# Kernel optimization log

Hardware: AMD Instinct MI355X
Metric: run time of the kernel (lower is better)

## Reference

```python
import jax, jax.numpy as jnp
import numpy as np

NEG_INF = -1.0e15  # matches the module's self.infty


def setup_inputs() -> dict:
    key = jax.random.key(0)
    ks = jax.random.split(key, 12)
    B, N, D, H, HD = 256, 1024, 128, 8, 16
    inp = {
        "x": jax.random.normal(ks[0], (B, N, D), dtype=jnp.float32),
        "h_g": jax.random.normal(ks[1], (B, D), dtype=jnp.float32),
        "first": jax.random.normal(ks[2], (B, D), dtype=jnp.float32),
        "last": jax.random.normal(ks[3], (B, D), dtype=jnp.float32),
        "context": jax.random.normal(ks[4], (B, 2), dtype=jnp.float32),
        "K": jax.random.normal(ks[5], (B, H, N, HD), dtype=jnp.float32),
        "V": jax.random.normal(ks[6], (B, H, N, HD), dtype=jnp.float32),
        "K_lg": jax.random.normal(ks[7], (B, N, D), dtype=jnp.float32),
        "Wq": jax.random.normal(ks[8], (D, 3 * D + 2), dtype=jnp.float32) * 0.05,
        "bq": jnp.zeros((D,), dtype=jnp.float32),
        "Wo": jax.random.normal(ks[9], (D, D), dtype=jnp.float32) * 0.05,
        "bo": jnp.zeros((D,), dtype=jnp.float32),
        "mask": jax.random.randint(ks[10], (B, N), 0, 2, dtype=jnp.int32),
        "t": 1,
    }
    return inp


def reference(x, h_g, first, last, context, K, V, K_lg, Wq, bq, Wo, bo, mask, t):
    B, N, D = x.shape
    H, HD = K.shape[1], K.shape[3]
    # t > 0 path: context vector from graph embedding + first/last visited nodes
    h_c = jnp.concatenate([h_g, first, last, context], axis=1)  # [B, 3D+2]
    Q = h_c @ Wq.T + bq                                          # [B, D]
    Q = Q.reshape(B, H, HD)                                      # single query per head
    # masked single-query multi-head attention
    scale = jnp.sqrt(jnp.asarray(HD, dtype=x.dtype))
    scores = jnp.einsum("bhd,bhnd->bhn", Q, K) / scale          # [B, H, N]
    scores = jnp.where(mask[:, None, :] == 0, NEG_INF, scores)
    attn = jax.nn.softmax(scores, axis=-1)
    u = jnp.einsum("bhn,bhnd->bhd", attn, V).reshape(B, D)       # [B, D]
    u = u @ Wo.T + bo
    # pointer logits with tanh clipping
    logits = jnp.einsum("bd,bnd->bn", u, K_lg) / jnp.sqrt(jnp.asarray(D, dtype=x.dtype))
    logits = 10.0 * jnp.tanh(logits)
    logits = jnp.where(mask == 0, NEG_INF, logits)
    p = jax.nn.softmax(logits, axis=1)                           # [B, N]
    vertexes = jnp.argmax(p, axis=1)[:, None]                    # greedy (sample=False)
    probs = jnp.take_along_axis(p, vertexes, axis=1)             # [B, 1]
    return vertexes, probs
```

## Files before the change

### kernel.cpp

```cpp
#include <hip/hip_runtime.h>
#include <math.h>

#define Bn 256
#define Nn 1024
#define Dn 128
#define Hn 8
#define HDn 16
#define NEG_INF -1.0e15f

__global__ __launch_bounds__(128) void k_q(
    const float* __restrict__ h_g, const float* __restrict__ first,
    const float* __restrict__ last, const float* __restrict__ context,
    const float* __restrict__ Wq, const float* __restrict__ bq,
    float* __restrict__ Qout)
{
    __shared__ __align__(16) float hc[3 * Dn + 2];
    const int b = blockIdx.x;
    const int t = threadIdx.x;
    hc[t]          = h_g[b * Dn + t];
    hc[Dn + t]     = first[b * Dn + t];
    hc[2 * Dn + t] = last[b * Dn + t];
    if (t < 2) hc[3 * Dn + t] = context[b * 2 + t];
    __syncthreads();

    const float2* w2 = (const float2*)(Wq + (size_t)t * (3 * Dn + 2));
    const float2* h2 = (const float2*)hc;
    float acc = bq[t];
#pragma unroll 8
    for (int k = 0; k < (3 * Dn + 2) / 2; ++k) {
        float2 w = w2[k], h = h2[k];
        acc = fmaf(w.x, h.x, fmaf(w.y, h.y, acc));
    }
    Qout[b * Dn + t] = acc;
}

__global__ __launch_bounds__(256) void k_attn(
    const float* __restrict__ Q, const float* __restrict__ K,
    const float* __restrict__ V, const int* __restrict__ mask,
    float* __restrict__ Uout)
{
    __shared__ float sQ[HDn];
    __shared__ __align__(16) int sM[Nn];
    __shared__ float sRed[4];
    __shared__ float sSum[4];
    __shared__ float sUp[4][HDn];

    const int bh = blockIdx.x;
    const int b = bh >> 3;
    const int tid = threadIdx.x;
    const int lane = tid & 63, wave = tid >> 6;
    const int d4 = tid & 3;
    const int g = tid >> 2;

    ((int4*)sM)[tid] = ((const int4*)(mask + (size_t)b * Nn))[tid];
    if (tid < HDn) sQ[tid] = Q[b * Dn + (bh & 7) * HDn + tid];
    __syncthreads();
    const float4 qf = ((const float4*)sQ)[d4];

    const float4* __restrict__ Kp = (const float4*)(K + (size_t)bh * Nn * HDn);
    const float4* __restrict__ Vp = (const float4*)(V + (size_t)bh * Nn * HDn);

    float4 kf[16], vf[16];
#pragma unroll
    for (int i = 0; i < 16; ++i) kf[i] = Kp[(size_t)(g + 64 * i) * 4 + d4];
#pragma unroll
    for (int i = 0; i < 16; ++i) vf[i] = Vp[(size_t)(g + 64 * i) * 4 + d4];
    __builtin_amdgcn_sched_barrier(0);

    float s[16];
    float lmax = NEG_INF;
#pragma unroll
    for (int i = 0; i < 16; ++i) {
        float p = qf.x * kf[i].x + qf.y * kf[i].y + qf.z * kf[i].z + qf.w * kf[i].w;
        p += __shfl_xor(p, 1, 64);
        p += __shfl_xor(p, 2, 64);
        p = (sM[g + 64 * i] == 0) ? NEG_INF : (p * 0.25f);
        s[i] = p;
        lmax = fmaxf(lmax, p);
    }
#pragma unroll
    for (int o = 4; o <= 32; o <<= 1) lmax = fmaxf(lmax, __shfl_xor(lmax, o, 64));
    if (lane == 0) sRed[wave] = lmax;
    __syncthreads();
    const float m = fmaxf(fmaxf(sRed[0], sRed[1]), fmaxf(sRed[2], sRed[3]));

    float lsum = 0.f;
    float4 acc = {0.f, 0.f, 0.f, 0.f};
#pragma unroll
    for (int i = 0; i < 16; ++i) {
        const float e = __expf(s[i] - m);
        lsum += e;
        acc.x = fmaf(e, vf[i].x, acc.x);
        acc.y = fmaf(e, vf[i].y, acc.y);
        acc.z = fmaf(e, vf[i].z, acc.z);
        acc.w = fmaf(e, vf[i].w, acc.w);
    }
#pragma unroll
    for (int o = 4; o <= 32; o <<= 1) {
        acc.x += __shfl_xor(acc.x, o, 64);
        acc.y += __shfl_xor(acc.y, o, 64);
        acc.z += __shfl_xor(acc.z, o, 64);
        acc.w += __shfl_xor(acc.w, o, 64);
        lsum  += __shfl_xor(lsum, o, 64);
    }
    if (lane < 4) {
        sUp[wave][lane * 4 + 0] = acc.x;
        sUp[wave][lane * 4 + 1] = acc.y;
        sUp[wave][lane * 4 + 2] = acc.z;
        sUp[wave][lane * 4 + 3] = acc.w;
    }
    if (lane == 0) sSum[wave] = lsum;
    __syncthreads();
    if (tid < HDn) {
        const float inv = 1.0f / (sSum[0] + sSum[1] + sSum[2] + sSum[3]);
        const float u = (sUp[0][tid] + sUp[1][tid] + sUp[2][tid] + sUp[3][tid]) * inv;
        Uout[b * Dn + (bh & 7) * HDn + tid] = u;
    }
}

__global__ __launch_bounds__(1024) void k_ptr(
    const float* __restrict__ U, const float* __restrict__ Wo,
    const float* __restrict__ bo, const float* __restrict__ K_lg,
    const int* __restrict__ mask, float* __restrict__ out)
{
    __shared__ __align__(16) float sU[Dn];
    __shared__ __align__(16) float sU2[Dn];
    __shared__ __align__(16) float sL[Nn];
    __shared__ float sRv[16];
    __shared__ int   sRi[16];
    __shared__ float sRs[16];

    const int b = blockIdx.x;
    const int tid = threadIdx.x;
    const int lane = tid & 63, wave = tid >> 6;

    if (tid < Dn) sU[tid] = U[b * Dn + tid];
    __syncthreads();
    {
        const int d = tid >> 3, e8 = tid & 7;
        const float4* wrow = (const float4*)(Wo + (size_t)d * Dn + e8 * 16);
        const float4* su4 = (const float4*)(sU + e8 * 16);
        float acc = 0.f;
#pragma unroll
        for (int k = 0; k < 4; ++k) {
            const float4 w = wrow[k], u = su4[k];
            acc = fmaf(w.x, u.x, fmaf(w.y, u.y, fmaf(w.z, u.z, fmaf(w.w, u.w, acc))));
        }
        acc += __shfl_xor(acc, 1, 64);
        acc += __shfl_xor(acc, 2, 64);
        acc += __shfl_xor(acc, 4, 64);
        if (e8 == 0) sU2[d] = acc + bo[d];
    }
    __syncthreads();

    const float4* __restrict__ Kl = (const float4*)(K_lg + (size_t)b * Nn * Dn);
    const int* __restrict__ mrow = mask + (size_t)b * Nn;
    const int grp = tid >> 5, l32 = tid & 31;
    const float4 u2f = ((const float4*)sU2)[l32];
    const float sc = 0.08838834764831845f;
#pragma unroll
    for (int it0 = 0; it0 < 32; it0 += 4) {
        float4 kl[4];
#pragma unroll
        for (int j = 0; j < 4; ++j)
            kl[j] = Kl[(size_t)(grp + 32 * (it0 + j)) * 32 + l32];
        __builtin_amdgcn_sched_barrier(0);
#pragma unroll
        for (int j = 0; j < 4; ++j) {
            float p = kl[j].x * u2f.x + kl[j].y * u2f.y + kl[j].z * u2f.z + kl[j].w * u2f.w;
#pragma unroll
            for (int o = 16; o >= 1; o >>= 1) p += __shfl_xor(p, o, 64);
            if (l32 == 0) {
                const int n = grp + 32 * (it0 + j);
                sL[n] = (mrow[n] == 0) ? NEG_INF : 10.0f * tanhf(p * sc);
            }
        }
    }
    __syncthreads();

    float bv = sL[tid]; int bi = tid;
#pragma unroll
    for (int o = 32; o >= 1; o >>= 1) {
        const float ov = __shfl_xor(bv, o, 64);
        const int oi = __shfl_xor(bi, o, 64);
        if (ov > bv || (ov == bv && oi < bi)) { bv = ov; bi = oi; }
    }
    if (lane == 0) { sRv[wave] = bv; sRi[wave] = bi; }
    __syncthreads();
    bv = sRv[0]; bi = sRi[0];
#pragma unroll
    for (int w = 1; w < 16; ++w) {
        const float ov = sRv[w]; const int oi = sRi[w];
        if (ov > bv || (ov == bv && oi < bi)) { bv = ov; bi = oi; }
    }

    float lsum = __expf(sL[tid] - bv);
#pragma unroll
    for (int o = 32; o >= 1; o >>= 1) lsum += __shfl_xor(lsum, o, 64);
    if (lane == 0) sRs[wave] = lsum;
    __syncthreads();
    if (tid == 0) {
        float tot = 0.f;
#pragma unroll
        for (int w = 0; w < 16; ++w) tot += sRs[w];
        out[b] = (float)bi;
        out[Bn + b] = 1.0f / tot;
    }
}

extern "C" void kernel_launch(void* const* d_in, const int* in_sizes, int n_in,
                              void* d_out, int out_size, void* d_ws, size_t ws_size,
                              hipStream_t stream) {
    const float* h_g     = (const float*)d_in[1];
    const float* first   = (const float*)d_in[2];
    const float* last    = (const float*)d_in[3];
    const float* context = (const float*)d_in[4];
    const float* K       = (const float*)d_in[5];
    const float* V       = (const float*)d_in[6];
    const float* K_lg    = (const float*)d_in[7];
    const float* Wq      = (const float*)d_in[8];
    const float* bq      = (const float*)d_in[9];
    const float* Wo      = (const float*)d_in[10];
    const float* bo      = (const float*)d_in[11];
    const int*   mask    = (const int*)d_in[12];
    float* out = (float*)d_out;

    float* Qws = (float*)d_ws;
    float* Uws = Qws + Bn * Dn;

    k_q   <<<Bn,      128, 0, stream>>>(h_g, first, last, context, Wq, bq, Qws);
    k_attn<<<Bn * Hn, 256, 0, stream>>>(Qws, K, V, mask, Uws);
    k_ptr <<<Bn,     1024, 0, stream>>>(Uws, Wo, bo, K_lg, mask, out);
}
```

Baseline: 113.2 us.

## Restructure attention kernel: thread-per-key rows, four heads per block, double-buffered loads

```diff
diff --git a/kernel.cpp b/kernel.cpp
--- a/kernel.cpp
+++ b/kernel.cpp
@@ -34,87 +34,106 @@
     Qout[b * Dn + t] = acc;
 }
 
-__global__ __launch_bounds__(256) void k_attn(
+__global__ __launch_bounds__(512, 4) void k_attn(
     const float* __restrict__ Q, const float* __restrict__ K,
     const float* __restrict__ V, const int* __restrict__ mask,
     float* __restrict__ Uout)
 {
-    __shared__ float sQ[HDn];
-    __shared__ __align__(16) int sM[Nn];
-    __shared__ float sRed[4];
+    __shared__ float sQ[64];
+    __shared__ float sPart[512][17];
+    __shared__ float sOut[64];
     __shared__ float sSum[4];
-    __shared__ float sUp[4][HDn];
-
-    const int bh = blockIdx.x;
-    const int b = bh >> 3;
+
+    const int blk = blockIdx.x;
+    const int b = blk >> 1, pr = blk & 1;
     const int tid = threadIdx.x;
-    const int lane = tid & 63, wave = tid >> 6;
-    const int d4 = tid & 3;
-    const int g = tid >> 2;
-
-    ((int4*)sM)[tid] = ((const int4*)(mask + (size_t)b * Nn))[tid];
-    if (tid < HDn) sQ[tid] = Q[b * Dn + (bh & 7) * HDn + tid];
-    __syncthreads();
-    const float4 qf = ((const float4*)sQ)[d4];
-
-    const float4* __restrict__ Kp = (const float4*)(K + (size_t)bh * Nn * HDn);
-    const float4* __restrict__ Vp = (const float4*)(V + (size_t)bh * Nn * HDn);
-
-    float4 kf[16], vf[16];
-#pragma unroll
-    for (int i = 0; i < 16; ++i) kf[i] = Kp[(size_t)(g + 64 * i) * 4 + d4];
-#pragma unroll
-    for (int i = 0; i < 16; ++i) vf[i] = Vp[(size_t)(g + 64 * i) * 4 + d4];
-    __builtin_amdgcn_sched_barrier(0);
-
-    float s[16];
-    float lmax = NEG_INF;
-#pragma unroll
-    for (int i = 0; i < 16; ++i) {
-        float p = qf.x * kf[i].x + qf.y * kf[i].y + qf.z * kf[i].z + qf.w * kf[i].w;
-        p += __shfl_xor(p, 1, 64);
-        p += __shfl_xor(p, 2, 64);
-        p = (sM[g + 64 * i] == 0) ? NEG_INF : (p * 0.25f);
-        s[i] = p;
-        lmax = fmaxf(lmax, p);
-    }
-#pragma unroll
-    for (int o = 4; o <= 32; o <<= 1) lmax = fmaxf(lmax, __shfl_xor(lmax, o, 64));
-    if (lane == 0) sRed[wave] = lmax;
-    __syncthreads();
-    const float m = fmaxf(fmaxf(sRed[0], sRed[1]), fmaxf(sRed[2], sRed[3]));
-
-    float lsum = 0.f;
-    float4 acc = {0.f, 0.f, 0.f, 0.f};
-#pragma unroll
-    for (int i = 0; i < 16; ++i) {
-        const float e = __expf(s[i] - m);
-        lsum += e;
-        acc.x = fmaf(e, vf[i].x, acc.x);
-        acc.y = fmaf(e, vf[i].y, acc.y);
-        acc.z = fmaf(e, vf[i].z, acc.z);
-        acc.w = fmaf(e, vf[i].w, acc.w);
-    }
-#pragma unroll
-    for (int o = 4; o <= 32; o <<= 1) {
-        acc.x += __shfl_xor(acc.x, o, 64);
-        acc.y += __shfl_xor(acc.y, o, 64);
-        acc.z += __shfl_xor(acc.z, o, 64);
-        acc.w += __shfl_xor(acc.w, o, 64);
-        lsum  += __shfl_xor(lsum, o, 64);
-    }
-    if (lane < 4) {
-        sUp[wave][lane * 4 + 0] = acc.x;
-        sUp[wave][lane * 4 + 1] = acc.y;
-        sUp[wave][lane * 4 + 2] = acc.z;
-        sUp[wave][lane * 4 + 3] = acc.w;
-    }
-    if (lane == 0) sSum[wave] = lsum;
-    __syncthreads();
-    if (tid < HDn) {
-        const float inv = 1.0f / (sSum[0] + sSum[1] + sSum[2] + sSum[3]);
-        const float u = (sUp[0][tid] + sUp[1][tid] + sUp[2][tid] + sUp[3][tid]) * inv;
-        Uout[b * Dn + (bh & 7) * HDn + tid] = u;
+    const int hl = tid >> 7;
+    const int h = pr * 4 + hl;
+    const int lh = tid & 127;
+
+    if (tid < 64) sQ[tid] = Q[b * Dn + pr * 64 + tid];
+
+    const int* __restrict__ mrow = mask + (size_t)b * Nn;
+    int mk[8];
+#pragma unroll
+    for (int i = 0; i < 8; ++i) mk[i] = mrow[lh + 128 * i];
+
+    __syncthreads();
+    float4 q4[4];
+#pragma unroll
+    for (int j = 0; j < 4; ++j) q4[j] = ((const float4*)(sQ + hl * 16))[j];
+
+    const float4* __restrict__ Kp = (const float4*)(K + ((size_t)b * Hn + h) * Nn * HDn);
+    const float4* __restrict__ Vp = (const float4*)(V + ((size_t)b * Hn + h) * Nn * HDn);
+
+    float4 kb[2][4], vb[2][4];
+#pragma unroll
+    for (int j = 0; j < 4; ++j) {
+        kb[0][j] = Kp[(size_t)lh * 4 + j];
+        vb[0][j] = Vp[(size_t)lh * 4 + j];
+    }
+
+    float4 u0 = {0,0,0,0}, u1 = {0,0,0,0}, u2 = {0,0,0,0}, u3 = {0,0,0,0};
+    float sum = 0.f;
+
+#pragma unroll
+    for (int i = 0; i < 8; ++i) {
+        const int cur = i & 1, nxt = cur ^ 1;
+        if (i < 7) {
+            const int n = lh + 128 * (i + 1);
+#pragma unroll
+            for (int j = 0; j < 4; ++j) {
+                kb[nxt][j] = Kp[(size_t)n * 4 + j];
+                vb[nxt][j] = Vp[(size_t)n * 4 + j];
+            }
+        }
+        __builtin_amdgcn_sched_barrier(0);
+        float s = 0.f;
+#pragma unroll
+        for (int j = 0; j < 4; ++j) {
+            s = fmaf(q4[j].x, kb[cur][j].x, s);
+            s = fmaf(q4[j].y, kb[cur][j].y, s);
+            s = fmaf(q4[j].z, kb[cur][j].z, s);
+            s = fmaf(q4[j].w, kb[cur][j].w, s);
+        }
+        const float e = mk[i] ? __expf(s * 0.25f) : 0.f;
+        sum += e;
+        u0.x = fmaf(e, vb[cur][0].x, u0.x); u0.y = fmaf(e, vb[cur][0].y, u0.y);
+        u0.z = fmaf(e, vb[cur][0].z, u0.z); u0.w = fmaf(e, vb[cur][0].w, u0.w);
+        u1.x = fmaf(e, vb[cur][1].x, u1.x); u1.y = fmaf(e, vb[cur][1].y, u1.y);
+        u1.z = fmaf(e, vb[cur][1].z, u1.z); u1.w = fmaf(e, vb[cur][1].w, u1.w);
+        u2.x = fmaf(e, vb[cur][2].x, u2.x); u2.y = fmaf(e, vb[cur][2].y, u2.y);
+        u2.z = fmaf(e, vb[cur][2].z, u2.z); u2.w = fmaf(e, vb[cur][2].w, u2.w);
+        u3.x = fmaf(e, vb[cur][3].x, u3.x); u3.y = fmaf(e, vb[cur][3].y, u3.y);
+        u3.z = fmaf(e, vb[cur][3].z, u3.z); u3.w = fmaf(e, vb[cur][3].w, u3.w);
+    }
+
+    {
+        float* p = sPart[tid];
+        p[0]=u0.x; p[1]=u0.y; p[2]=u0.z; p[3]=u0.w;
+        p[4]=u1.x; p[5]=u1.y; p[6]=u1.z; p[7]=u1.w;
+        p[8]=u2.x; p[9]=u2.y; p[10]=u2.z; p[11]=u2.w;
+        p[12]=u3.x; p[13]=u3.y; p[14]=u3.z; p[15]=u3.w;
+        p[16]=sum;
+    }
+    __syncthreads();
+
+    if (tid < 64) {
+        const int hh = tid >> 4, d = tid & 15;
+        float a = 0.f;
+#pragma unroll 8
+        for (int j = 0; j < 128; ++j) a += sPart[hh * 128 + j][d];
+        sOut[tid] = a;
+    } else if (tid < 68) {
+        const int hh = tid - 64;
+        float a = 0.f;
+#pragma unroll 8
+        for (int j = 0; j < 128; ++j) a += sPart[hh * 128 + j][16];
+        sSum[hh] = a;
+    }
+    __syncthreads();
+    if (tid < 64) {
+        Uout[b * Dn + pr * 64 + tid] = sOut[tid] / sSum[tid >> 4];
     }
 }
 
@@ -229,6 +248,6 @@
     float* Uws = Qws + Bn * Dn;
 
     k_q   <<<Bn,      128, 0, stream>>>(h_g, first, last, context, Wq, bq, Qws);
-    k_attn<<<Bn * Hn, 256, 0, stream>>>(Qws, K, V, mask, Uws);
+    k_attn<<<Bn * 2,  512, 0, stream>>>(Qws, K, V, mask, Uws);
     k_ptr <<<Bn,     1024, 0, stream>>>(Uws, Wo, bo, K_lg, mask, out);
 }
```

Result: slower. 117.4 us (+3.7%).

## Stream K/V through double-buffered LDS via global_load_lds in attention kernel

Applied to the files above, without the earlier changes.

```diff
diff --git a/kernel.cpp b/kernel.cpp
--- a/kernel.cpp
+++ b/kernel.cpp
@@ -7,6 +7,15 @@
 #define Hn 8
 #define HDn 16
 #define NEG_INF -1.0e15f
+
+#define AS(n) __attribute__((address_space(n)))
+#define WAITV(n) asm volatile("s_waitcnt vmcnt(" #n ")" ::: "memory")
+
+__device__ __forceinline__ void gl_lds16(const float* g, float* l) {
+    __builtin_amdgcn_global_load_lds(
+        (AS(1) void*)(unsigned long long)g,
+        (AS(3) void*)l, 16, 0, 0);
+}
 
 __global__ __launch_bounds__(128) void k_q(
     const float* __restrict__ h_g, const float* __restrict__ first,
@@ -39,82 +48,95 @@
     const float* __restrict__ V, const int* __restrict__ mask,
     float* __restrict__ Uout)
 {
-    __shared__ float sQ[HDn];
-    __shared__ __align__(16) int sM[Nn];
-    __shared__ float sRed[4];
-    __shared__ float sSum[4];
-    __shared__ float sUp[4][HDn];
+    __shared__ __align__(16) float sK[2 * 2048];
+    __shared__ __align__(16) float sV[2 * 2048];
+    __shared__ __align__(16) float sP[16 * 4];
+    __shared__ float sS[4];
 
     const int bh = blockIdx.x;
-    const int b = bh >> 3;
+    const int b = bh >> 3, h = bh & 7;
     const int tid = threadIdx.x;
     const int lane = tid & 63, wave = tid >> 6;
-    const int d4 = tid & 3;
-    const int g = tid >> 2;
-
-    ((int4*)sM)[tid] = ((const int4*)(mask + (size_t)b * Nn))[tid];
-    if (tid < HDn) sQ[tid] = Q[b * Dn + (bh & 7) * HDn + tid];
-    __syncthreads();
-    const float4 qf = ((const float4*)sQ)[d4];
-
-    const float4* __restrict__ Kp = (const float4*)(K + (size_t)bh * Nn * HDn);
-    const float4* __restrict__ Vp = (const float4*)(V + (size_t)bh * Nn * HDn);
-
-    float4 kf[16], vf[16];
-#pragma unroll
-    for (int i = 0; i < 16; ++i) kf[i] = Kp[(size_t)(g + 64 * i) * 4 + d4];
-#pragma unroll
-    for (int i = 0; i < 16; ++i) vf[i] = Vp[(size_t)(g + 64 * i) * 4 + d4];
+    const int g = tid & 3;
+    const int kq = tid >> 2;
+
+    const int* __restrict__ mrow = mask + (size_t)b * Nn;
+    int mk[16];
+#pragma unroll
+    for (int c = 0; c < 8; ++c) {
+        mk[c * 2]     = mrow[c * 128 + kq];
+        mk[c * 2 + 1] = mrow[c * 128 + 64 + kq];
+    }
+    const float4 qg = ((const float4*)(Q + (size_t)b * Dn + h * HDn))[g];
+    WAITV(0);
     __builtin_amdgcn_sched_barrier(0);
 
-    float s[16];
-    float lmax = NEG_INF;
-#pragma unroll
-    for (int i = 0; i < 16; ++i) {
-        float p = qf.x * kf[i].x + qf.y * kf[i].y + qf.z * kf[i].z + qf.w * kf[i].w;
-        p += __shfl_xor(p, 1, 64);
-        p += __shfl_xor(p, 2, 64);
-        p = (sM[g + 64 * i] == 0) ? NEG_INF : (p * 0.25f);
-        s[i] = p;
-        lmax = fmaxf(lmax, p);
-    }
-#pragma unroll
-    for (int o = 4; o <= 32; o <<= 1) lmax = fmaxf(lmax, __shfl_xor(lmax, o, 64));
-    if (lane == 0) sRed[wave] = lmax;
-    __syncthreads();
-    const float m = fmaxf(fmaxf(sRed[0], sRed[1]), fmaxf(sRed[2], sRed[3]));
-
-    float lsum = 0.f;
-    float4 acc = {0.f, 0.f, 0.f, 0.f};
-#pragma unroll
-    for (int i = 0; i < 16; ++i) {
-        const float e = __expf(s[i] - m);
-        lsum += e;
-        acc.x = fmaf(e, vf[i].x, acc.x);
-        acc.y = fmaf(e, vf[i].y, acc.y);
-        acc.z = fmaf(e, vf[i].z, acc.z);
-        acc.w = fmaf(e, vf[i].w, acc.w);
-    }
+    const float4* __restrict__ Kg = (const float4*)(K + (size_t)bh * Nn * HDn);
+    const float4* __restrict__ Vg = (const float4*)(V + (size_t)bh * Nn * HDn);
+
+#define STAGE(c, buf) {                                                       \
+    gl_lds16((const float*)(Kg + (c) * 512 + tid),       sK + (buf) * 2048 + tid * 4);        \
+    gl_lds16((const float*)(Kg + (c) * 512 + 256 + tid), sK + (buf) * 2048 + 1024 + tid * 4); \
+    gl_lds16((const float*)(Vg + (c) * 512 + tid),       sV + (buf) * 2048 + tid * 4);        \
+    gl_lds16((const float*)(Vg + (c) * 512 + 256 + tid), sV + (buf) * 2048 + 1024 + tid * 4); \
+}
+
+    STAGE(0, 0);
+    STAGE(1, 1);
+
+    float4 u = {0.f, 0.f, 0.f, 0.f};
+    float sum = 0.f;
+
+#pragma unroll
+    for (int c = 0; c < 8; ++c) {
+        if (c < 7) { WAITV(4); } else { WAITV(0); }
+        __builtin_amdgcn_sched_barrier(0);
+        __builtin_amdgcn_s_barrier();
+        const float* kb = sK + (c & 1) * 2048;
+        const float* vb = sV + (c & 1) * 2048;
+#pragma unroll
+        for (int kk = 0; kk < 2; ++kk) {
+            const int key = kq + 64 * kk;
+            const float4 kf = *(const float4*)(kb + key * 16 + g * 4);
+            const float4 vf = *(const float4*)(vb + key * 16 + g * 4);
+            float p = qg.x * kf.x + qg.y * kf.y + qg.z * kf.z + qg.w * kf.w;
+            p += __shfl_xor(p, 1, 64);
+            p += __shfl_xor(p, 2, 64);
+            const float e = mk[c * 2 + kk] ? __expf(p * 0.25f) : 0.f;
+            sum += e;
+            u.x = fmaf(e, vf.x, u.x);
+            u.y = fmaf(e, vf.y, u.y);
+            u.z = fmaf(e, vf.z, u.z);
+            u.w = fmaf(e, vf.w, u.w);
+        }
+        __builtin_amdgcn_s_barrier();
+        if (c < 6) STAGE(c + 2, c & 1);
+    }
+#undef STAGE
+
 #pragma unroll
     for (int o = 4; o <= 32; o <<= 1) {
-        acc.x += __shfl_xor(acc.x, o, 64);
-        acc.y += __shfl_xor(acc.y, o, 64);
-        acc.z += __shfl_xor(acc.z, o, 64);
-        acc.w += __shfl_xor(acc.w, o, 64);
-        lsum  += __shfl_xor(lsum, o, 64);
-    }
-    if (lane < 4) {
-        sUp[wave][lane * 4 + 0] = acc.x;
-        sUp[wave][lane * 4 + 1] = acc.y;
-        sUp[wave][lane * 4 + 2] = acc.z;
-        sUp[wave][lane * 4 + 3] = acc.w;
-    }
-    if (lane == 0) sSum[wave] = lsum;
-    __syncthreads();
-    if (tid < HDn) {
-        const float inv = 1.0f / (sSum[0] + sSum[1] + sSum[2] + sSum[3]);
-        const float u = (sUp[0][tid] + sUp[1][tid] + sUp[2][tid] + sUp[3][tid]) * inv;
-        Uout[b * Dn + (bh & 7) * HDn + tid] = u;
+        u.x += __shfl_xor(u.x, o, 64);
+        u.y += __shfl_xor(u.y, o, 64);
+        u.z += __shfl_xor(u.z, o, 64);
+        u.w += __shfl_xor(u.w, o, 64);
+        sum += __shfl_xor(sum, o, 64);
+    }
+    if (lane < 4) ((float4*)sP)[wave * 4 + lane] = u;
+    if (lane == 0) sS[wave] = sum;
+    __syncthreads();
+    if (tid < 4) {
+        const float4 t0 = ((const float4*)sP)[0 * 4 + tid];
+        const float4 t1 = ((const float4*)sP)[1 * 4 + tid];
+        const float4 t2 = ((const float4*)sP)[2 * 4 + tid];
+        const float4 t3 = ((const float4*)sP)[3 * 4 + tid];
+        const float inv = 1.0f / (sS[0] + sS[1] + sS[2] + sS[3]);
+        float4 r;
+        r.x = (t0.x + t1.x + t2.x + t3.x) * inv;
+        r.y = (t0.y + t1.y + t2.y + t3.y) * inv;
+        r.z = (t0.z + t1.z + t2.z + t3.z) * inv;
+        r.w = (t0.w + t1.w + t2.w + t3.w) * inv;
+        ((float4*)(Uout + (size_t)b * Dn + h * HDn))[tid] = r;
     }
 }
 
```

Result: no change. 113.6 us (+0.3%).

## Restructure attention to one block per batch and drop softmax max pass

Applied to the files above, without the earlier changes.

```diff
diff --git a/kernel.cpp b/kernel.cpp
--- a/kernel.cpp
+++ b/kernel.cpp
@@ -7,6 +7,8 @@
 #define Hn 8
 #define HDn 16
 #define NEG_INF -1.0e15f
+
+typedef float v4f __attribute__((ext_vector_type(4)));
 
 __global__ __launch_bounds__(128) void k_q(
     const float* __restrict__ h_g, const float* __restrict__ first,
@@ -34,87 +36,80 @@
     Qout[b * Dn + t] = acc;
 }
 
-__global__ __launch_bounds__(256) void k_attn(
+__global__ __launch_bounds__(1024) void k_attn(
     const float* __restrict__ Q, const float* __restrict__ K,
     const float* __restrict__ V, const int* __restrict__ mask,
     float* __restrict__ Uout)
 {
-    __shared__ float sQ[HDn];
-    __shared__ __align__(16) int sM[Nn];
-    __shared__ float sRed[4];
-    __shared__ float sSum[4];
-    __shared__ float sUp[4][HDn];
-
-    const int bh = blockIdx.x;
-    const int b = bh >> 3;
+    __shared__ __align__(16) float sPart[16][Hn][20];
+    __shared__ __align__(16) float sTot[Hn][20];
+
+    const int b = blockIdx.x;
     const int tid = threadIdx.x;
     const int lane = tid & 63, wave = tid >> 6;
-    const int d4 = tid & 3;
-    const int g = tid >> 2;
-
-    ((int4*)sM)[tid] = ((const int4*)(mask + (size_t)b * Nn))[tid];
-    if (tid < HDn) sQ[tid] = Q[b * Dn + (bh & 7) * HDn + tid];
-    __syncthreads();
-    const float4 qf = ((const float4*)sQ)[d4];
-
-    const float4* __restrict__ Kp = (const float4*)(K + (size_t)bh * Nn * HDn);
-    const float4* __restrict__ Vp = (const float4*)(V + (size_t)bh * Nn * HDn);
-
-    float4 kf[16], vf[16];
-#pragma unroll
-    for (int i = 0; i < 16; ++i) kf[i] = Kp[(size_t)(g + 64 * i) * 4 + d4];
-#pragma unroll
-    for (int i = 0; i < 16; ++i) vf[i] = Vp[(size_t)(g + 64 * i) * 4 + d4];
-    __builtin_amdgcn_sched_barrier(0);
-
-    float s[16];
-    float lmax = NEG_INF;
-#pragma unroll
-    for (int i = 0; i < 16; ++i) {
-        float p = qf.x * kf[i].x + qf.y * kf[i].y + qf.z * kf[i].z + qf.w * kf[i].w;
-        p += __shfl_xor(p, 1, 64);
-        p += __shfl_xor(p, 2, 64);
-        p = (sM[g + 64 * i] == 0) ? NEG_INF : (p * 0.25f);
-        s[i] = p;
-        lmax = fmaxf(lmax, p);
-    }
-#pragma unroll
-    for (int o = 4; o <= 32; o <<= 1) lmax = fmaxf(lmax, __shfl_xor(lmax, o, 64));
-    if (lane == 0) sRed[wave] = lmax;
-    __syncthreads();
-    const float m = fmaxf(fmaxf(sRed[0], sRed[1]), fmaxf(sRed[2], sRed[3]));
-
-    float lsum = 0.f;
-    float4 acc = {0.f, 0.f, 0.f, 0.f};
-#pragma unroll
-    for (int i = 0; i < 16; ++i) {
-        const float e = __expf(s[i] - m);
-        lsum += e;
-        acc.x = fmaf(e, vf[i].x, acc.x);
-        acc.y = fmaf(e, vf[i].y, acc.y);
-        acc.z = fmaf(e, vf[i].z, acc.z);
-        acc.w = fmaf(e, vf[i].w, acc.w);
-    }
-#pragma unroll
-    for (int o = 4; o <= 32; o <<= 1) {
-        acc.x += __shfl_xor(acc.x, o, 64);
-        acc.y += __shfl_xor(acc.y, o, 64);
-        acc.z += __shfl_xor(acc.z, o, 64);
-        acc.w += __shfl_xor(acc.w, o, 64);
-        lsum  += __shfl_xor(lsum, o, 64);
-    }
-    if (lane < 4) {
-        sUp[wave][lane * 4 + 0] = acc.x;
-        sUp[wave][lane * 4 + 1] = acc.y;
-        sUp[wave][lane * 4 + 2] = acc.z;
-        sUp[wave][lane * 4 + 3] = acc.w;
-    }
-    if (lane == 0) sSum[wave] = lsum;
-    __syncthreads();
-    if (tid < HDn) {
-        const float inv = 1.0f / (sSum[0] + sSum[1] + sSum[2] + sSum[3]);
-        const float u = (sUp[0][tid] + sUp[1][tid] + sUp[2][tid] + sUp[3][tid]) * inv;
-        Uout[b * Dn + (bh & 7) * HDn + tid] = u;
+    const int g = tid & 3;
+    const int kq = tid >> 2;
+
+    const int* __restrict__ mrow = mask + (size_t)b * Nn;
+    int mk[4];
+#pragma unroll
+    for (int p = 0; p < 4; ++p) mk[p] = mrow[p * 256 + kq];
+
+    const float4* __restrict__ Qrow = (const float4*)(Q + (size_t)b * Dn);
+    const float4* __restrict__ Kb = (const float4*)(K + (size_t)b * Hn * Nn * HDn);
+    const float4* __restrict__ Vb = (const float4*)(V + (size_t)b * Hn * Nn * HDn);
+
+#pragma unroll
+    for (int s = 0; s < Hn; ++s) {
+        const float4 qg = Qrow[s * 4 + g];
+        const float4* __restrict__ Kh = Kb + (size_t)s * 4096;
+        const float4* __restrict__ Vh = Vb + (size_t)s * 4096;
+
+        float4 kf[4], vf[4];
+#pragma unroll
+        for (int p = 0; p < 4; ++p) kf[p] = Kh[p * 1024 + tid];
+#pragma unroll
+        for (int p = 0; p < 4; ++p) vf[p] = Vh[p * 1024 + tid];
+        __builtin_amdgcn_sched_barrier(0);
+
+        float4 u = {0.f, 0.f, 0.f, 0.f};
+        float sum = 0.f;
+#pragma unroll
+        for (int p = 0; p < 4; ++p) {
+            float sc = qg.x * kf[p].x + qg.y * kf[p].y + qg.z * kf[p].z + qg.w * kf[p].w;
+            sc += __shfl_xor(sc, 1, 64);
+            sc += __shfl_xor(sc, 2, 64);
+            const float e = mk[p] ? __expf(sc * 0.25f) : 0.f;
+            sum += e;
+            u.x = fmaf(e, vf[p].x, u.x);
+            u.y = fmaf(e, vf[p].y, u.y);
+            u.z = fmaf(e, vf[p].z, u.z);
+            u.w = fmaf(e, vf[p].w, u.w);
+        }
+#pragma unroll
+        for (int o = 4; o <= 32; o <<= 1) {
+            u.x += __shfl_xor(u.x, o, 64);
+            u.y += __shfl_xor(u.y, o, 64);
+            u.z += __shfl_xor(u.z, o, 64);
+            u.w += __shfl_xor(u.w, o, 64);
+            sum += __shfl_xor(sum, o, 64);
+        }
+        if (lane < 4) *(float4*)(&sPart[wave][s][lane * 4]) = u;
+        if (lane == 0) sPart[wave][s][16] = sum;
+    }
+    __syncthreads();
+
+    if (tid < Hn * 17) {
+        const int s = tid / 17, j = tid % 17;
+        float a = 0.f;
+#pragma unroll
+        for (int w = 0; w < 16; ++w) a += sPart[w][s][j];
+        sTot[s][j] = a;
+    }
+    __syncthreads();
+    if (tid < Dn) {
+        const int s = tid >> 4, j = tid & 15;
+        Uout[(size_t)b * Dn + tid] = sTot[s][j] / sTot[s][16];
     }
 }
 
@@ -153,17 +148,17 @@
     }
     __syncthreads();
 
-    const float4* __restrict__ Kl = (const float4*)(K_lg + (size_t)b * Nn * Dn);
+    const v4f* __restrict__ Kl = (const v4f*)(K_lg + (size_t)b * Nn * Dn);
     const int* __restrict__ mrow = mask + (size_t)b * Nn;
     const int grp = tid >> 5, l32 = tid & 31;
-    const float4 u2f = ((const float4*)sU2)[l32];
+    const v4f u2f = ((const v4f*)sU2)[l32];
     const float sc = 0.08838834764831845f;
 #pragma unroll
     for (int it0 = 0; it0 < 32; it0 += 4) {
-        float4 kl[4];
+        v4f kl[4];
 #pragma unroll
         for (int j = 0; j < 4; ++j)
-            kl[j] = Kl[(size_t)(grp + 32 * (it0 + j)) * 32 + l32];
+            kl[j] = __builtin_nontemporal_load(&Kl[(size_t)(grp + 32 * (it0 + j)) * 32 + l32]);
         __builtin_amdgcn_sched_barrier(0);
 #pragma unroll
         for (int j = 0; j < 4; ++j) {
@@ -228,7 +223,7 @@
     float* Qws = (float*)d_ws;
     float* Uws = Qws + Bn * Dn;
 
-    k_q   <<<Bn,      128, 0, stream>>>(h_g, first, last, context, Wq, bq, Qws);
-    k_attn<<<Bn * Hn, 256, 0, stream>>>(Qws, K, V, mask, Uws);
-    k_ptr <<<Bn,     1024, 0, stream>>>(Uws, Wo, bo, K_lg, mask, out);
-}
+    k_q   <<<Bn,  128, 0, stream>>>(h_g, first, last, context, Wq, bq, Qws);
+    k_attn<<<Bn, 1024, 0, stream>>>(Qws, K, V, mask, Uws);
+    k_ptr <<<Bn, 1024, 0, stream>>>(Uws, Wo, bo, K_lg, mask, out);
+}
```

Result: faster. 106.6 us (-5.9%).
